# Kernel optimization log

Measured on AMD Instinct MI355X. Metric: run time of the kernel, lower is better.

Reference implementation:

```python
import jax, jax.numpy as jnp
import numpy as np

EPS = 1e-5  # BatchNorm eps

def _bn(x):
    # BatchNorm1d(affine=False) in training mode: per-agent, per-feature batch stats
    m = jnp.mean(x, axis=1, keepdims=True)
    v = jnp.var(x, axis=1, keepdims=True)
    return (x - m) / jnp.sqrt(v + EPS)

def _lrelu(x):
    return jax.nn.leaky_relu(x, 0.01)

def setup_inputs() -> dict:
    key = jax.random.key(0)
    ks = jax.random.split(key, 14)
    A, B, IN, OUT, H, K = 8, 32768, 128, 32, 128, 4
    D = H // K
    s = 0.05
    return {
        "states": jax.random.normal(ks[0], (A, B, IN), jnp.float32),
        "actions": jax.random.normal(ks[1], (A, B, OUT), jnp.float32),
        "enc_w": jax.random.normal(ks[2], (A, IN + OUT, H), jnp.float32) * s,
        "enc_b": jax.random.normal(ks[3], (A, H), jnp.float32) * s,
        "aenc_w": jax.random.normal(ks[4], (A, OUT, H), jnp.float32) * s,
        "aenc_b": jax.random.normal(ks[5], (A, H), jnp.float32) * s,
        "key_w": jax.random.normal(ks[6], (K, H, D), jnp.float32) * s,
        "sel_w": jax.random.normal(ks[7], (K, H, D), jnp.float32) * s,
        "val_w": jax.random.normal(ks[8], (K, H, D), jnp.float32) * s,
        "val_b": jax.random.normal(ks[9], (K, D), jnp.float32) * s,
        "c1_w": jax.random.normal(ks[10], (A, 2 * H, H), jnp.float32) * s,
        "c1_b": jax.random.normal(ks[11], (A, H), jnp.float32) * s,
        "c2_w": jax.random.normal(ks[12], (A, H, 1), jnp.float32) * s,
        "c2_b": jax.random.normal(ks[13], (A, 1), jnp.float32) * s,
    }

def reference(states, actions, enc_w, enc_b, aenc_w, aenc_b,
              key_w, sel_w, val_w, val_b, c1_w, c1_b, c2_w, c2_b):
    A, B, _ = states.shape
    # per-agent state-action encodings: [A,B,H]
    sa = _bn(jnp.concatenate([states, actions], axis=-1))
    sa_enc = _lrelu(jnp.einsum('abi,aih->abh', sa, enc_w) + enc_b[:, None, :])
    # per-agent action encodings: [A,B,H]
    a_in = _bn(actions)
    a_enc = _lrelu(jnp.einsum('abi,aih->abh', a_in, aenc_w) + aenc_b[:, None, :])
    # per-head keys/values/selectors: [K,A,B,D]
    keys = jnp.einsum('abh,khd->kabd', a_enc, key_w)
    vals = _lrelu(jnp.einsum('abh,khd->kabd', a_enc, val_w) + val_b[:, None, None, :])
    sels = jnp.einsum('abh,khd->kabd', sa_enc, sel_w)
    D = keys.shape[-1]
    # attention logits over other agents: [K,B,A_query,A_key], self excluded
    logits = jnp.einsum('kibd,kjbd->kbij', sels, keys) / jnp.sqrt(jnp.float32(D))
    self_mask = jnp.eye(A, dtype=bool)[None, None]
    probs = jax.nn.softmax(jnp.where(self_mask, -jnp.inf, logits), axis=-1)
    # attended values: [K,A,B,D] -> concat heads -> [A,B,K*D]
    other = jnp.einsum('kbij,kjbd->kibd', probs, vals)
    other_cat = jnp.transpose(other, (1, 2, 0, 3)).reshape(A, B, -1)
    # per-agent critics on [sa_enc, attended]: [A,B,1]
    critic_in = jnp.concatenate([sa_enc, other_cat], axis=-1)
    h = _lrelu(jnp.einsum('abi,aih->abh', critic_in, c1_w) + c1_b[:, None, :])
    q = jnp.einsum('abh,aho->abo', h, c2_w) + c2_b[:, None, :]
    return q
```

## Files before the change

kernel.cpp:

```cpp
#include <hip/hip_runtime.h>
#include <hip/hip_bf16.h>
#include <stdint.h>

#define A_N 8
#define B_N 32768
#define IN_N 128
#define OUT_N 32
#define SAF 160
#define H_N 128
#define D_N 32
#define KD_N 128
#define CIN_N 256
#define CHUNKS 128
#define EPSV 1e-5f

typedef unsigned int u32;
typedef unsigned short u16;
typedef __attribute__((ext_vector_type(8))) short short8;
typedef __attribute__((ext_vector_type(4))) float floatx4;

typedef __attribute__((address_space(1))) void gvoid;
typedef __attribute__((address_space(3))) void lvoid;
__device__ __forceinline__ void glds16(const void* g, void* l){
  __builtin_amdgcn_global_load_lds((gvoid*)g, (lvoid*)l, 16, 0, 0);
}

__device__ __forceinline__ int swzu(int u){ return u ^ ((u >> 3) & 3); }
__device__ __forceinline__ int swzi(int rr){
  int u = rr >> 3;
  u ^= (u >> 3) & 3;
  return (u << 3) | (rr & 7);
}

__device__ __forceinline__ float bf_lo(u32 u){ return __uint_as_float(u << 16); }
__device__ __forceinline__ float bf_hi(u32 u){ return __uint_as_float(u & 0xffff0000u); }
__device__ __forceinline__ float bf2f(u16 b){ return __uint_as_float(((u32)b) << 16); }
__device__ __forceinline__ u16 f2bf(float f){
  u32 u = __float_as_uint(f);
  return (u16)((u + 0x7fffu + ((u >> 16) & 1u)) >> 16);
}
__device__ __forceinline__ float lrelu(float x){ return x > 0.f ? x : 0.01f * x; }

__global__ __launch_bounds__(256) void k_stats(
    const float* __restrict__ states, const float* __restrict__ actions,
    float* __restrict__ part)
{
  int a = blockIdx.y;
  int chunk = blockIdx.x;
  int t = threadIdx.x;
  int r0 = chunk * (B_N / CHUNKS);
  __shared__ float red[512];
  {
    int f = t & 127, half = t >> 7;
    const float* p = states + ((size_t)a * B_N + r0 + half) * IN_N + f;
    float s1 = 0.f, s2 = 0.f;
    for (int it = 0; it < 128; ++it){
      float v = p[(size_t)(2 * it) * IN_N];
      s1 += v; s2 += v * v;
    }
    red[t] = s1; red[256 + t] = s2;
    __syncthreads();
    if (t < 128){
      float a1 = red[t] + red[t + 128];
      float a2 = red[256 + t] + red[256 + t + 128];
      size_t o = (((size_t)a * CHUNKS + chunk) * SAF + t) * 2;
      part[o] = a1; part[o + 1] = a2;
    }
    __syncthreads();
  }
  {
    int f = t & 31, g = t >> 5;
    const float* p = actions + ((size_t)a * B_N + r0 + g) * OUT_N + f;
    float s1 = 0.f, s2 = 0.f;
    for (int it = 0; it < 32; ++it){
      float v = p[(size_t)(8 * it) * OUT_N];
      s1 += v; s2 += v * v;
    }
    red[t] = s1; red[256 + t] = s2;
    __syncthreads();
    if (t < 32){
      float a1 = 0.f, a2 = 0.f;
      #pragma unroll
      for (int gg = 0; gg < 8; ++gg){
        a1 += red[t + 32 * gg];
        a2 += red[256 + t + 32 * gg];
      }
      size_t o = (((size_t)a * CHUNKS + chunk) * SAF + 128 + t) * 2;
      part[o] = a1; part[o + 1] = a2;
    }
  }
}

__global__ void k_finalize(const float* __restrict__ part,
                           float* __restrict__ meanArr, float* __restrict__ istdArr)
{
  int idx = blockIdx.x * blockDim.x + threadIdx.x;
  if (idx >= A_N * SAF) return;
  int a = idx / SAF, f = idx % SAF;
  float s1 = 0.f, s2 = 0.f;
  for (int c = 0; c < CHUNKS; ++c){
    size_t o = (((size_t)a * CHUNKS + c) * SAF + f) * 2;
    s1 += part[o]; s2 += part[o + 1];
  }
  float m = s1 * (1.f / B_N);
  float v = s2 * (1.f / B_N) - m * m;
  if (v < 0.f) v = 0.f;
  meanArr[idx] = m;
  istdArr[idx] = rsqrtf(v + EPSV);
}

__device__ __forceinline__ void packpair(float w, u16* __restrict__ dh,
                                         u16* __restrict__ dl, int i){
  u16 h = f2bf(w);
  dh[i] = h;
  dl[i] = f2bf(w - bf2f(h));
}

__global__ __launch_bounds__(256) void k_pack(
    const float* __restrict__ enc_w, const float* __restrict__ aenc_w,
    const float* __restrict__ key_w, const float* __restrict__ sel_w,
    const float* __restrict__ val_w, const float* __restrict__ c1_w,
    u16* __restrict__ encH, u16* __restrict__ encL,
    u16* __restrict__ aencH, u16* __restrict__ aencL,
    u16* __restrict__ keyH, u16* __restrict__ selH, u16* __restrict__ valH,
    u16* __restrict__ c1H, u16* __restrict__ c1L)
{
  int i = blockIdx.x * 256 + threadIdx.x;
  const int S0 = A_N * H_N * SAF;
  const int S1 = A_N * H_N * OUT_N;
  const int S2 = KD_N * H_N;
  const int S5 = A_N * H_N * CIN_N;
  if (i < S0){
    int a = i / (H_N * SAF); int r = i % (H_N * SAF);
    int tile = r >> 12; int rr = r & 4095;
    int n = rr >> 5; int kk = rr & 31;
    int kg = tile * 32 + kk;
    int d = (i & ~4095) | swzi(rr);
    packpair(enc_w[((size_t)a * SAF + kg) * H_N + n], encH, encL, d);
    return;
  }
  i -= S0;
  if (i < S1){
    int a = i >> 12; int rr = i & 4095;
    int n = rr >> 5; int k = rr & 31;
    int d = (i & ~4095) | swzi(rr);
    packpair(aenc_w[((size_t)a * OUT_N + k) * H_N + n], aencH, aencL, d);
    return;
  }
  i -= S1;
  if (i < 3 * S2){
    int which = i / S2; int j = i % S2;
    int tile = j >> 12; int rr = j & 4095;
    int n = rr >> 5; int kk = rr & 31;
    int kg = tile * 32 + kk;
    const float* w = (which == 0) ? key_w : ((which == 1) ? sel_w : val_w);
    u16* dh = (which == 0) ? keyH : ((which == 1) ? selH : valH);
    dh[(j & ~4095) | swzi(rr)] =
        f2bf(w[(((size_t)(n >> 5)) * H_N + kg) * D_N + (n & 31)]);
    return;
  }
  i -= 3 * S2;
  if (i < S5){
    int a = i >> 15; int r = i & 32767;
    int tile = r >> 12; int rr = r & 4095;
    int n = rr >> 5; int kk = rr & 31;
    int kg = tile * 32 + kk;
    int d = (i & ~4095) | swzi(rr);
    packpair(c1_w[((size_t)a * CIN_N + kg) * H_N + n], c1H, c1L, d);
  }
}
#define PACK_TOTAL (A_N*H_N*SAF + A_N*H_N*OUT_N + 3*KD_N*H_N + A_N*H_N*CIN_N)

__global__ __launch_bounds__(256, 3) void k_enc_sel(
    const float* __restrict__ states, const float* __restrict__ actions,
    const float* __restrict__ mean, const float* __restrict__ istd,
    const u16* __restrict__ encH, const u16* __restrict__ encL,
    const float* __restrict__ enc_b,
    const u16* __restrict__ selH,
    u16* __restrict__ sa_enc, u16* __restrict__ sels)
{
  int a = blockIdx.y; int row0 = blockIdx.x * 128; int t = threadIdx.x;
  int lane = t & 63, wave = t >> 6, l16 = lane & 15, quad = lane >> 4;
  __shared__ __align__(16) u16 S[25600];
  __shared__ __align__(16) float sc[160], sh[160];
  u16* Wh = S;
  u16* Wl = S + 4096;
  u16* Xh = S + 8192;
  u16* Xl = S + 13312;
  u16* T  = S;
  u16* Ws = S + 17408;

  if (t < SAF){
    float m = mean[a * SAF + t], s = istd[a * SAF + t];
    sc[t] = s; sh[t] = -m * s;
  }
  floatx4 acc[2][8];
  #pragma unroll
  for (int mt = 0; mt < 2; ++mt)
    #pragma unroll
    for (int nt = 0; nt < 8; ++nt) acc[mt][nt] = (floatx4){0.f,0.f,0.f,0.f};
  const u16* ebh = encH + (size_t)a * (H_N * SAF);
  const u16* ebl = encL + (size_t)a * (H_N * SAF);
  __syncthreads();

  for (int k0 = 0; k0 < SAF; k0 += 32){
    const u16* th = ebh + (k0 >> 5) * 4096;
    const u16* tl = ebl + (k0 >> 5) * 4096;
    #pragma unroll
    for (int c = t; c < 512; c += 256){
      glds16(th + c * 8, Wh + c * 8);
      glds16(tl + c * 8, Wl + c * 8);
    }
    for (int c = t; c < 1024; c += 256){
      int r = c >> 3, kc = (c & 7) * 4, f = k0 + kc;
      size_t row = (size_t)a * B_N + row0 + r;
      float4 v;
      if (f < IN_N) v = *(const float4*)(states + row * IN_N + f);
      else          v = *(const float4*)(actions + row * OUT_N + (f - IN_N));
      float4 scv = *(const float4*)&sc[f];
      float4 shv = *(const float4*)&sh[f];
      float x0 = fmaf(v.x, scv.x, shv.x), x1 = fmaf(v.y, scv.y, shv.y);
      float x2 = fmaf(v.z, scv.z, shv.z), x3 = fmaf(v.w, scv.w, shv.w);
      u16 h0 = f2bf(x0), h1 = f2bf(x1), h2 = f2bf(x2), h3 = f2bf(x3);
      uint2 hv; hv.x = (u32)h0 | ((u32)h1 << 16); hv.y = (u32)h2 | ((u32)h3 << 16);
      *(uint2*)&Xh[r * 40 + kc] = hv;
      u16 l0 = f2bf(x0 - bf2f(h0)), l1 = f2bf(x1 - bf2f(h1));
      u16 l2 = f2bf(x2 - bf2f(h2)), l3 = f2bf(x3 - bf2f(h3));
      uint2 lv; lv.x = (u32)l0 | ((u32)l1 << 16); lv.y = (u32)l2 | ((u32)l3 << 16);
      *(uint2*)&Xl[r * 40 + kc] = lv;
    }
    __syncthreads();
    {
      short8 ah[2], al[2], bh[8], bl[8];
      #pragma unroll
      for (int mt = 0; mt < 2; ++mt){
        int rr = (wave * 32 + mt * 16 + l16) * 40 + quad * 8;
        ah[mt] = *(const short8*)&Xh[rr];
        al[mt] = *(const short8*)&Xl[rr];
      }
      #pragma unroll
      for (int nt = 0; nt < 8; ++nt){
        int v = (nt * 16 + l16) * 4 + quad; v ^= (v >> 3) & 3;
        bh[nt] = *(const short8*)&Wh[v * 8];
        bl[nt] = *(const short8*)&Wl[v * 8];
      }
      #pragma unroll
      for (int mt = 0; mt < 2; ++mt)
        #pragma unroll
        for (int nt = 0; nt < 8; ++nt){
          acc[mt][nt] = __builtin_amdgcn_mfma_f32_16x16x32_bf16(ah[mt], bh[nt], acc[mt][nt], 0,0,0);
          acc[mt][nt] = __builtin_amdgcn_mfma_f32_16x16x32_bf16(ah[mt], bl[nt], acc[mt][nt], 0,0,0);
          acc[mt][nt] = __builtin_amdgcn_mfma_f32_16x16x32_bf16(al[mt], bh[nt], acc[mt][nt], 0,0,0);
        }
    }
    __syncthreads();
  }

  {
    float bv[8];
    #pragma unroll
    for (int nt = 0; nt < 8; ++nt) bv[nt] = enc_b[a * H_N + nt * 16 + l16];
    #pragma unroll
    for (int mt = 0; mt < 2; ++mt)
      #pragma unroll
      for (int nt = 0; nt < 8; ++nt)
        #pragma unroll
        for (int r = 0; r < 4; ++r){
          int rl = wave * 32 + mt * 16 + quad * 4 + r;
          T[rl * 136 + nt * 16 + l16] = f2bf(lrelu(acc[mt][nt][r] + bv[nt]));
        }
  }
  __syncthreads();
  for (int c = t; c < 2048; c += 256){
    int row = c >> 4, col8 = (c & 15) * 8;
    *(uint4*)(sa_enc + ((size_t)a * B_N + row0 + row) * H_N + col8) =
        *(const uint4*)&T[row * 136 + col8];
  }

  #pragma unroll
  for (int mt = 0; mt < 2; ++mt)
    #pragma unroll
    for (int nt = 0; nt < 8; ++nt) acc[mt][nt] = (floatx4){0.f,0.f,0.f,0.f};
  for (int k0 = 0; k0 < H_N; k0 += 64){
    #pragma unroll
    for (int c = t; c < 1024; c += 256)
      glds16(selH + (k0 >> 5) * 4096 + c * 8, Ws + c * 8);
    __syncthreads();
    #pragma unroll
    for (int ks = 0; ks < 64; ks += 32){
      short8 ah[2], bh[8];
      #pragma unroll
      for (int mt = 0; mt < 2; ++mt)
        ah[mt] = *(const short8*)&T[(wave * 32 + mt * 16 + l16) * 136 + k0 + ks + quad * 8];
      #pragma unroll
      for (int nt = 0; nt < 8; ++nt){
        int v = ((ks >> 5) << 9) + (nt * 16 + l16) * 4 + quad; v ^= (v >> 3) & 3;
        bh[nt] = *(const short8*)&Ws[v * 8];
      }
      #pragma unroll
      for (int mt = 0; mt < 2; ++mt)
        #pragma unroll
        for (int nt = 0; nt < 8; ++nt)
          acc[mt][nt] = __builtin_amdgcn_mfma_f32_16x16x32_bf16(ah[mt], bh[nt], acc[mt][nt], 0,0,0);
    }
    __syncthreads();
  }
  #pragma unroll
  for (int mt = 0; mt < 2; ++mt)
    #pragma unroll
    for (int nt = 0; nt < 8; ++nt)
      #pragma unroll
      for (int r = 0; r < 4; ++r){
        int rl = wave * 32 + mt * 16 + quad * 4 + r;
        T[rl * 136 + nt * 16 + l16] = f2bf(acc[mt][nt][r]);
      }
  __syncthreads();
  for (int c = t; c < 2048; c += 256){
    int row = c >> 4, col8 = (c & 15) * 8;
    *(uint4*)(sels + ((size_t)a * B_N + row0 + row) * H_N + col8) =
        *(const uint4*)&T[row * 136 + col8];
  }
}

__global__ __launch_bounds__(256, 2) void k_aenc_kv(
    const float* __restrict__ actions,
    const float* __restrict__ mean, const float* __restrict__ istd,
    const u16* __restrict__ aencH, const u16* __restrict__ aencL,
    const float* __restrict__ aenc_b,
    const u16* __restrict__ keyH, const u16* __restrict__ valH,
    const float* __restrict__ val_b,
    u16* __restrict__ keys, u16* __restrict__ vals)
{
  int a = blockIdx.y; int row0 = blockIdx.x * 128; int t = threadIdx.x;
  int lane = t & 63, wave = t >> 6, l16 = lane & 15, quad = lane >> 4;
  __shared__ __align__(16) u16 S[34816];
  __shared__ __align__(16) float sc[32], sh[32];
  u16* T  = S;
  u16* WK = S + 17408;
  u16* WV = S + 25600;
  u16* T2 = S + 17408;

  if (t < 32){
    float m = mean[a * SAF + 128 + t], s = istd[a * SAF + 128 + t];
    sc[t] = s; sh[t] = -m * s;
  }
  floatx4 accK[2][8], accV[2][8];
  #pragma unroll
  for (int mt = 0; mt < 2; ++mt)
    #pragma unroll
    for (int nt = 0; nt < 8; ++nt){
      accK[mt][nt] = (floatx4){0.f,0.f,0.f,0.f};
      accV[mt][nt] = (floatx4){0.f,0.f,0.f,0.f};
    }
  __syncthreads();

  {
    u16* Wh1 = S;  u16* Wl1 = S + 4096;
    u16* Xh = S + 8192; u16* Xl = S + 13312;
    const u16* abh = aencH + (size_t)a * 4096;
    const u16* abl = aencL + (size_t)a * 4096;
    #pragma unroll
    for (int c = t; c < 512; c += 256){
      glds16(abh + c * 8, Wh1 + c * 8);
      glds16(abl + c * 8, Wl1 + c * 8);
    }
    for (int c = t; c < 1024; c += 256){
      int r = c >> 3, kc = (c & 7) * 4;
      size_t row = (size_t)a * B_N + row0 + r;
      float4 v = *(const float4*)(actions + row * OUT_N + kc);
      float4 scv = *(const float4*)&sc[kc];
      float4 shv = *(const float4*)&sh[kc];
      float x0 = fmaf(v.x, scv.x, shv.x), x1 = fmaf(v.y, scv.y, shv.y);
      float x2 = fmaf(v.z, scv.z, shv.z), x3 = fmaf(v.w, scv.w, shv.w);
      u16 h0 = f2bf(x0), h1 = f2bf(x1), h2 = f2bf(x2), h3 = f2bf(x3);
      uint2 hv; hv.x = (u32)h0 | ((u32)h1 << 16); hv.y = (u32)h2 | ((u32)h3 << 16);
      *(uint2*)&Xh[r * 40 + kc] = hv;
      u16 l0 = f2bf(x0 - bf2f(h0)), l1 = f2bf(x1 - bf2f(h1));
      u16 l2 = f2bf(x2 - bf2f(h2)), l3 = f2bf(x3 - bf2f(h3));
      uint2 lv; lv.x = (u32)l0 | ((u32)l1 << 16); lv.y = (u32)l2 | ((u32)l3 << 16);
      *(uint2*)&Xl[r * 40 + kc] = lv;
    }
    __syncthreads();
    short8 ah[2], al[2], bh[8], bl[8];
    #pragma unroll
    for (int mt = 0; mt < 2; ++mt){
      int rr = (wave * 32 + mt * 16 + l16) * 40 + quad * 8;
      ah[mt] = *(const short8*)&Xh[rr];
      al[mt] = *(const short8*)&Xl[rr];
    }
    #pragma unroll
    for (int nt = 0; nt < 8; ++nt){
      int v = (nt * 16 + l16) * 4 + quad; v ^= (v >> 3) & 3;
      bh[nt] = *(const short8*)&Wh1[v * 8];
      bl[nt] = *(const short8*)&Wl1[v * 8];
    }
    #pragma unroll
    for (int mt = 0; mt < 2; ++mt)
      #pragma unroll
      for (int nt = 0; nt < 8; ++nt){
        accK[mt][nt] = __builtin_amdgcn_mfma_f32_16x16x32_bf16(ah[mt], bh[nt], accK[mt][nt], 0,0,0);
        accK[mt][nt] = __builtin_amdgcn_mfma_f32_16x16x32_bf16(ah[mt], bl[nt], accK[mt][nt], 0,0,0);
        accK[mt][nt] = __builtin_amdgcn_mfma_f32_16x16x32_bf16(al[mt], bh[nt], accK[mt][nt], 0,0,0);
      }
    __syncthreads();
  }
  {
    float bv[8];
    #pragma unroll
    for (int nt = 0; nt < 8; ++nt) bv[nt] = aenc_b[a * H_N + nt * 16 + l16];
    #pragma unroll
    for (int mt = 0; mt < 2; ++mt)
      #pragma unroll
      for (int nt = 0; nt < 8; ++nt){
        #pragma unroll
        for (int r = 0; r < 4; ++r){
          int rl = wave * 32 + mt * 16 + quad * 4 + r;
          T[rl * 136 + nt * 16 + l16] = f2bf(lrelu(accK[mt][nt][r] + bv[nt]));
        }
        accK[mt][nt] = (floatx4){0.f,0.f,0.f,0.f};
      }
  }

  for (int k0 = 0; k0 < H_N; k0 += 64){
    __syncthreads();
    #pragma unroll
    for (int c = t; c < 1024; c += 256){
      glds16(keyH + (k0 >> 5) * 4096 + c * 8, WK + c * 8);
      glds16(valH + (k0 >> 5) * 4096 + c * 8, WV + c * 8);
    }
    __syncthreads();
    #pragma unroll
    for (int ks = 0; ks < 64; ks += 32){
      short8 ah[2], bk[8], bv[8];
      #pragma unroll
      for (int mt = 0; mt < 2; ++mt)
        ah[mt] = *(const short8*)&T[(wave * 32 + mt * 16 + l16) * 136 + k0 + ks + quad * 8];
      #pragma unroll
      for (int nt = 0; nt < 8; ++nt){
        int v = ((ks >> 5) << 9) + (nt * 16 + l16) * 4 + quad; v ^= (v >> 3) & 3;
        bk[nt] = *(const short8*)&WK[v * 8];
        bv[nt] = *(const short8*)&WV[v * 8];
      }
      #pragma unroll
      for (int mt = 0; mt < 2; ++mt)
        #pragma unroll
        for (int nt = 0; nt < 8; ++nt){
          accK[mt][nt] = __builtin_amdgcn_mfma_f32_16x16x32_bf16(ah[mt], bk[nt], accK[mt][nt], 0,0,0);
          accV[mt][nt] = __builtin_amdgcn_mfma_f32_16x16x32_bf16(ah[mt], bv[nt], accV[mt][nt], 0,0,0);
        }
    }
  }
  __syncthreads();
  {
    float bv[8];
    #pragma unroll
    for (int nt = 0; nt < 8; ++nt) bv[nt] = val_b[nt * 16 + l16];
    #pragma unroll
    for (int mt = 0; mt < 2; ++mt)
      #pragma unroll
      for (int nt = 0; nt < 8; ++nt)
        #pragma unroll
        for (int r = 0; r < 4; ++r){
          int rl = wave * 32 + mt * 16 + quad * 4 + r;
          T[rl * 136 + nt * 16 + l16]  = f2bf(lrelu(accV[mt][nt][r] + bv[nt]));
          T2[rl * 136 + nt * 16 + l16] = f2bf(accK[mt][nt][r]);
        }
  }
  __syncthreads();
  for (int c = t; c < 2048; c += 256){
    int row = c >> 4, col8 = (c & 15) * 8;
    *(uint4*)(vals + ((size_t)a * B_N + row0 + row) * H_N + col8) =
        *(const uint4*)&T[row * 136 + col8];
    *(uint4*)(keys + ((size_t)a * B_N + row0 + row) * H_N + col8) =
        *(const uint4*)&T2[row * 136 + col8];
  }
}

__global__ __launch_bounds__(256) void k_attn(
    const u16* __restrict__ sels, const u16* __restrict__ keys,
    const u16* __restrict__ vals, u16* __restrict__ other)
{
  int b0 = blockIdx.x * 8;
  int t = threadIdx.x;
  __shared__ __align__(16) u16 sS[8192], sK[8192], sV[8192];
  #pragma unroll
  for (int c = t; c < 1024; c += 256){
    int pr = c >> 4, uir = c & 15;
    int aa = pr & 7, bl2 = pr >> 3;
    int kk = uir >> 2, dg = uir & 3;
    int U = (bl2 * 4 + dg) * 32 + kk * 8 + (aa ^ (kk << 1) ^ dg);
    size_t go = ((size_t)aa * B_N + b0 + bl2) * KD_N;
    ((uint4*)sS)[U] = *((const uint4*)(sels + go) + uir);
    ((uint4*)sK)[U] = *((const uint4*)(keys + go) + uir);
    ((uint4*)sV)[U] = *((const uint4*)(vals + go) + uir);
  }
  __syncthreads();
  int i = t & 7, k = (t >> 3) & 3, bl = t >> 5;
  float si[32];
  #pragma unroll
  for (int dg = 0; dg < 4; ++dg){
    int U = (bl * 4 + dg) * 32 + k * 8 + (i ^ (k << 1) ^ dg);
    uint4 s4 = ((const uint4*)sS)[U];
    const u32* sp = (const u32*)&s4;
    #pragma unroll
    for (int jj = 0; jj < 4; ++jj){
      int d2 = dg * 4 + jj;
      si[2 * d2] = bf_lo(sp[jj]); si[2 * d2 + 1] = bf_hi(sp[jj]);
    }
  }
  float lg[8];
  #pragma unroll
  for (int j = 0; j < 8; ++j){
    float acc = 0.f;
    #pragma unroll
    for (int dg = 0; dg < 4; ++dg){
      int U = (bl * 4 + dg) * 32 + k * 8 + (j ^ (k << 1) ^ dg);
      uint4 k4 = ((const uint4*)sK)[U];
      const u32* kp = (const u32*)&k4;
      #pragma unroll
      for (int jj = 0; jj < 4; ++jj){
        int d2 = dg * 4 + jj;
        acc = fmaf(si[2 * d2], bf_lo(kp[jj]), acc);
        acc = fmaf(si[2 * d2 + 1], bf_hi(kp[jj]), acc);
      }
    }
    lg[j] = acc * 0.17677669529663689f;
  }
  float mx = -3.0e38f;
  #pragma unroll
  for (int j = 0; j < 8; ++j) if (j != i) mx = fmaxf(mx, lg[j]);
  float pe[8], se = 0.f;
  #pragma unroll
  for (int j = 0; j < 8; ++j){
    pe[j] = (j == i) ? 0.f : __expf(lg[j] - mx);
    se += pe[j];
  }
  float inv = 1.f / se;
  #pragma unroll
  for (int j = 0; j < 8; ++j) pe[j] *= inv;
  float o0[16], o1[16];
  #pragma unroll
  for (int d2 = 0; d2 < 16; ++d2){ o0[d2] = 0.f; o1[d2] = 0.f; }
  #pragma unroll
  for (int j = 0; j < 8; ++j){
    #pragma unroll
    for (int dg = 0; dg < 4; ++dg){
      int U = (bl * 4 + dg) * 32 + k * 8 + (j ^ (k << 1) ^ dg);
      uint4 v4 = ((const uint4*)sV)[U];
      const u32* vp = (const u32*)&v4;
      #pragma unroll
      for (int jj = 0; jj < 4; ++jj){
        int d2 = dg * 4 + jj;
        o0[d2] = fmaf(pe[j], bf_lo(vp[jj]), o0[d2]);
        o1[d2] = fmaf(pe[j], bf_hi(vp[jj]), o1[d2]);
      }
    }
  }
  __align__(16) u16 ob[32];
  #pragma unroll
  for (int d2 = 0; d2 < 16; ++d2){
    ob[2 * d2] = f2bf(o0[d2]); ob[2 * d2 + 1] = f2bf(o1[d2]);
  }
  uint4* dst = (uint4*)(other + ((size_t)i * B_N + (b0 + bl)) * KD_N + k * 32);
  const uint4* s4o = (const uint4*)ob;
  #pragma unroll
  for (int c = 0; c < 4; ++c) dst[c] = s4o[c];
}

__global__ __launch_bounds__(256, 3) void k_critic(
    const u16* __restrict__ sa_enc, const u16* __restrict__ other,
    const u16* __restrict__ c1H, const u16* __restrict__ c1L,
    const float* __restrict__ c1_b,
    const float* __restrict__ c2w, const float* __restrict__ c2b,
    float* __restrict__ qout)
{
  int a = blockIdx.y; int row0 = blockIdx.x * 128; int t = threadIdx.x;
  int lane = t & 63, wave = t >> 6, l16 = lane & 15, quad = lane >> 4;
  __shared__ __align__(16) u16 Xs[4096];
  __shared__ __align__(16) u16 Wh[4096];
  __shared__ __align__(16) u16 Wl[4096];
  floatx4 acc[2][8];
  #pragma unroll
  for (int mt = 0; mt < 2; ++mt)
    #pragma unroll
    for (int nt = 0; nt < 8; ++nt) acc[mt][nt] = (floatx4){0.f,0.f,0.f,0.f};
  const u16* wbh = c1H + (size_t)a * (H_N * CIN_N);
  const u16* wbl = c1L + (size_t)a * (H_N * CIN_N);

  for (int kt = 0; kt < 8; ++kt){
    const u16* th = wbh + kt * 4096;
    const u16* tl = wbl + kt * 4096;
    #pragma unroll
    for (int c = t; c < 512; c += 256){
      glds16(th + c * 8, Wh + c * 8);
      glds16(tl + c * 8, Wl + c * 8);
    }
    {
      const u16* src = (kt < 4) ? sa_enc : other;
      int kb = (kt < 4) ? kt * 32 : kt * 32 - H_N;
      #pragma unroll
      for (int c = t; c < 512; c += 256){
        int r = c >> 2, off = (c & 3) * 8;
        glds16(src + ((size_t)a * B_N + row0 + r) * H_N + kb + off, Xs + c * 8);
      }
    }
    __syncthreads();
    {
      short8 ah[2], bh[8], bl[8];
      #pragma unroll
      for (int mt = 0; mt < 2; ++mt)
        ah[mt] = *(const short8*)&Xs[(wave * 32 + mt * 16 + l16) * 32 + quad * 8];
      #pragma unroll
      for (int nt = 0; nt < 8; ++nt){
        int v = (nt * 16 + l16) * 4 + quad; v ^= (v >> 3) & 3;
        bh[nt] = *(const short8*)&Wh[v * 8];
        bl[nt] = *(const short8*)&Wl[v * 8];
      }
      #pragma unroll
      for (int mt = 0; mt < 2; ++mt)
        #pragma unroll
        for (int nt = 0; nt < 8; ++nt){
          acc[mt][nt] = __builtin_amdgcn_mfma_f32_16x16x32_bf16(ah[mt], bh[nt], acc[mt][nt], 0,0,0);
          acc[mt][nt] = __builtin_amdgcn_mfma_f32_16x16x32_bf16(ah[mt], bl[nt], acc[mt][nt], 0,0,0);
        }
    }
    __syncthreads();
  }

  float c2r[8], bv[8];
  #pragma unroll
  for (int nt = 0; nt < 8; ++nt){
    c2r[nt] = c2w[a * H_N + nt * 16 + l16];
    bv[nt]  = c1_b[a * H_N + nt * 16 + l16];
  }
  #pragma unroll
  for (int mt = 0; mt < 2; ++mt){
    #pragma unroll
    for (int r = 0; r < 4; ++r){
      float s = 0.f;
      #pragma unroll
      for (int nt = 0; nt < 8; ++nt){
        float h = lrelu(acc[mt][nt][r] + bv[nt]);
        s = fmaf(h, c2r[nt], s);
      }
      s += __shfl_xor(s, 1);
      s += __shfl_xor(s, 2);
      s += __shfl_xor(s, 4);
      s += __shfl_xor(s, 8);
      if (l16 == 0){
        int row = row0 + wave * 32 + mt * 16 + quad * 4 + r;
        qout[(size_t)a * B_N + row] = s + c2b[a];
      }
    }
  }
}

extern "C" void kernel_launch(void* const* d_in, const int* in_sizes, int n_in,
                              void* d_out, int out_size, void* d_ws, size_t ws_size,
                              hipStream_t stream)
{
  const float* states  = (const float*)d_in[0];
  const float* actions = (const float*)d_in[1];
  const float* enc_w   = (const float*)d_in[2];
  const float* enc_b   = (const float*)d_in[3];
  const float* aenc_w  = (const float*)d_in[4];
  const float* aenc_b  = (const float*)d_in[5];
  const float* key_w   = (const float*)d_in[6];
  const float* sel_w   = (const float*)d_in[7];
  const float* val_w   = (const float*)d_in[8];
  const float* val_b   = (const float*)d_in[9];
  const float* c1_w    = (const float*)d_in[10];
  const float* c1_b    = (const float*)d_in[11];
  const float* c2_w    = (const float*)d_in[12];
  const float* c2_b    = (const float*)d_in[13];
  float* q = (float*)d_out;

  char* ws = (char*)d_ws;
  u16* encH  = (u16*)(ws + 0);
  u16* encL  = (u16*)(ws + 327680);
  u16* aencH = (u16*)(ws + 655360);
  u16* aencL = (u16*)(ws + 720896);
  u16* keyH  = (u16*)(ws + 786432);
  u16* selH  = (u16*)(ws + 819200);
  u16* valH  = (u16*)(ws + 851968);
  float* part    = (float*)ws;
  float* meanArr = (float*)(ws + 1310720);
  float* istdArr = (float*)(ws + 1315840);
  u16* c1H = (u16*)(ws + 1320960);
  u16* c1L = (u16*)(ws + 1845248);
  const size_t ibase = 4194304;
  const size_t BUF = (size_t)A_N * B_N * 128 * 2;
  u16* sa_enc = (u16*)(ws + ibase);
  u16* sels   = (u16*)(ws + ibase + BUF);
  u16* keys   = (u16*)(ws + ibase + 2 * BUF);
  u16* vals   = (u16*)(ws + ibase + 3 * BUF);

  k_stats<<<dim3(CHUNKS, A_N), 256, 0, stream>>>(states, actions, part);
  k_finalize<<<(A_N * SAF + 255) / 256, 256, 0, stream>>>(part, meanArr, istdArr);
  k_pack<<<(PACK_TOTAL + 255) / 256, 256, 0, stream>>>(
      enc_w, aenc_w, key_w, sel_w, val_w, c1_w,
      encH, encL, aencH, aencL, keyH, selH, valH, c1H, c1L);

  dim3 g(B_N / 128, A_N);
  k_enc_sel<<<g, 256, 0, stream>>>(states, actions, meanArr, istdArr,
                                   encH, encL, enc_b, selH, sa_enc, sels);
  k_aenc_kv<<<g, 256, 0, stream>>>(actions, meanArr, istdArr,
                                   aencH, aencL, aenc_b, keyH, valH, val_b,
                                   keys, vals);
  k_attn<<<B_N / 8, 256, 0, stream>>>(sels, keys, vals, keys);
  k_critic<<<g, 256, 0, stream>>>(sa_enc, keys, c1H, c1L, c1_b, c2_w, c2_b, q);
}
```

Baseline: 509.5 us.

## Drop weight LDS swizzle, shrink aenc_kv LDS, widen critic blocks to 512 threads

```diff
diff --git a/kernel.cpp b/kernel.cpp
--- a/kernel.cpp
+++ b/kernel.cpp
@@ -23,13 +23,6 @@
 typedef __attribute__((address_space(3))) void lvoid;
 __device__ __forceinline__ void glds16(const void* g, void* l){
   __builtin_amdgcn_global_load_lds((gvoid*)g, (lvoid*)l, 16, 0, 0);
-}
-
-__device__ __forceinline__ int swzu(int u){ return u ^ ((u >> 3) & 3); }
-__device__ __forceinline__ int swzi(int rr){
-  int u = rr >> 3;
-  u ^= (u >> 3) & 3;
-  return (u << 3) | (rr & 7);
 }
 
 __device__ __forceinline__ float bf_lo(u32 u){ return __uint_as_float(u << 16); }
@@ -135,16 +128,14 @@
     int tile = r >> 12; int rr = r & 4095;
     int n = rr >> 5; int kk = rr & 31;
     int kg = tile * 32 + kk;
-    int d = (i & ~4095) | swzi(rr);
-    packpair(enc_w[((size_t)a * SAF + kg) * H_N + n], encH, encL, d);
+    packpair(enc_w[((size_t)a * SAF + kg) * H_N + n], encH, encL, i);
     return;
   }
   i -= S0;
   if (i < S1){
     int a = i >> 12; int rr = i & 4095;
     int n = rr >> 5; int k = rr & 31;
-    int d = (i & ~4095) | swzi(rr);
-    packpair(aenc_w[((size_t)a * OUT_N + k) * H_N + n], aencH, aencL, d);
+    packpair(aenc_w[((size_t)a * OUT_N + k) * H_N + n], aencH, aencL, i);
     return;
   }
   i -= S1;
@@ -155,8 +146,7 @@
     int kg = tile * 32 + kk;
     const float* w = (which == 0) ? key_w : ((which == 1) ? sel_w : val_w);
     u16* dh = (which == 0) ? keyH : ((which == 1) ? selH : valH);
-    dh[(j & ~4095) | swzi(rr)] =
-        f2bf(w[(((size_t)(n >> 5)) * H_N + kg) * D_N + (n & 31)]);
+    dh[j] = f2bf(w[(((size_t)(n >> 5)) * H_N + kg) * D_N + (n & 31)]);
     return;
   }
   i -= 3 * S2;
@@ -165,8 +155,7 @@
     int tile = r >> 12; int rr = r & 4095;
     int n = rr >> 5; int kk = rr & 31;
     int kg = tile * 32 + kk;
-    int d = (i & ~4095) | swzi(rr);
-    packpair(c1_w[((size_t)a * CIN_N + kg) * H_N + n], c1H, c1L, d);
+    packpair(c1_w[((size_t)a * CIN_N + kg) * H_N + n], c1H, c1L, i);
   }
 }
 #define PACK_TOTAL (A_N*H_N*SAF + A_N*H_N*OUT_N + 3*KD_N*H_N + A_N*H_N*CIN_N)
@@ -240,9 +229,9 @@
       }
       #pragma unroll
       for (int nt = 0; nt < 8; ++nt){
-        int v = (nt * 16 + l16) * 4 + quad; v ^= (v >> 3) & 3;
-        bh[nt] = *(const short8*)&Wh[v * 8];
-        bl[nt] = *(const short8*)&Wl[v * 8];
+        int rr = (nt * 16 + l16) * 32 + quad * 8;
+        bh[nt] = *(const short8*)&Wh[rr];
+        bl[nt] = *(const short8*)&Wl[rr];
       }
       #pragma unroll
       for (int mt = 0; mt < 2; ++mt)
@@ -293,10 +282,8 @@
       for (int mt = 0; mt < 2; ++mt)
         ah[mt] = *(const short8*)&T[(wave * 32 + mt * 16 + l16) * 136 + k0 + ks + quad * 8];
       #pragma unroll
-      for (int nt = 0; nt < 8; ++nt){
-        int v = ((ks >> 5) << 9) + (nt * 16 + l16) * 4 + quad; v ^= (v >> 3) & 3;
-        bh[nt] = *(const short8*)&Ws[v * 8];
-      }
+      for (int nt = 0; nt < 8; ++nt)
+        bh[nt] = *(const short8*)&Ws[((ks >> 5) << 12) + (nt * 16 + l16) * 32 + quad * 8];
       #pragma unroll
       for (int mt = 0; mt < 2; ++mt)
         #pragma unroll
@@ -322,7 +309,7 @@
   }
 }
 
-__global__ __launch_bounds__(256, 2) void k_aenc_kv(
+__global__ __launch_bounds__(256, 3) void k_aenc_kv(
     const float* __restrict__ actions,
     const float* __restrict__ mean, const float* __restrict__ istd,
     const u16* __restrict__ aencH, const u16* __restrict__ aencL,
@@ -333,12 +320,11 @@
 {
   int a = blockIdx.y; int row0 = blockIdx.x * 128; int t = threadIdx.x;
   int lane = t & 63, wave = t >> 6, l16 = lane & 15, quad = lane >> 4;
-  __shared__ __align__(16) u16 S[34816];
+  __shared__ __align__(16) u16 S[25600];
   __shared__ __align__(16) float sc[32], sh[32];
   u16* T  = S;
   u16* WK = S + 17408;
-  u16* WV = S + 25600;
-  u16* T2 = S + 17408;
+  u16* WV = S + 21504;
 
   if (t < 32){
     float m = mean[a * SAF + 128 + t], s = istd[a * SAF + 128 + t];
@@ -390,9 +376,9 @@
     }
     #pragma unroll
     for (int nt = 0; nt < 8; ++nt){
-      int v = (nt * 16 + l16) * 4 + quad; v ^= (v >> 3) & 3;
-      bh[nt] = *(const short8*)&Wh1[v * 8];
-      bl[nt] = *(const short8*)&Wl1[v * 8];
+      int rr = (nt * 16 + l16) * 32 + quad * 8;
+      bh[nt] = *(const short8*)&Wh1[rr];
+      bl[nt] = *(const short8*)&Wl1[rr];
     }
     #pragma unroll
     for (int mt = 0; mt < 2; ++mt)
@@ -421,25 +407,24 @@
       }
   }
 
-  for (int k0 = 0; k0 < H_N; k0 += 64){
-    __syncthreads();
-    #pragma unroll
-    for (int c = t; c < 1024; c += 256){
+  for (int k0 = 0; k0 < H_N; k0 += 32){
+    __syncthreads();
+    #pragma unroll
+    for (int c = t; c < 512; c += 256){
       glds16(keyH + (k0 >> 5) * 4096 + c * 8, WK + c * 8);
       glds16(valH + (k0 >> 5) * 4096 + c * 8, WV + c * 8);
     }
     __syncthreads();
-    #pragma unroll
-    for (int ks = 0; ks < 64; ks += 32){
+    {
       short8 ah[2], bk[8], bv[8];
       #pragma unroll
       for (int mt = 0; mt < 2; ++mt)
-        ah[mt] = *(const short8*)&T[(wave * 32 + mt * 16 + l16) * 136 + k0 + ks + quad * 8];
+        ah[mt] = *(const short8*)&T[(wave * 32 + mt * 16 + l16) * 136 + k0 + quad * 8];
       #pragma unroll
       for (int nt = 0; nt < 8; ++nt){
-        int v = ((ks >> 5) << 9) + (nt * 16 + l16) * 4 + quad; v ^= (v >> 3) & 3;
-        bk[nt] = *(const short8*)&WK[v * 8];
-        bv[nt] = *(const short8*)&WV[v * 8];
+        int rr = (nt * 16 + l16) * 32 + quad * 8;
+        bk[nt] = *(const short8*)&WK[rr];
+        bv[nt] = *(const short8*)&WV[rr];
       }
       #pragma unroll
       for (int mt = 0; mt < 2; ++mt)
@@ -462,8 +447,7 @@
         #pragma unroll
         for (int r = 0; r < 4; ++r){
           int rl = wave * 32 + mt * 16 + quad * 4 + r;
-          T[rl * 136 + nt * 16 + l16]  = f2bf(lrelu(accV[mt][nt][r] + bv[nt]));
-          T2[rl * 136 + nt * 16 + l16] = f2bf(accK[mt][nt][r]);
+          T[rl * 136 + nt * 16 + l16] = f2bf(lrelu(accV[mt][nt][r] + bv[nt]));
         }
   }
   __syncthreads();
@@ -471,8 +455,22 @@
     int row = c >> 4, col8 = (c & 15) * 8;
     *(uint4*)(vals + ((size_t)a * B_N + row0 + row) * H_N + col8) =
         *(const uint4*)&T[row * 136 + col8];
+  }
+  __syncthreads();
+  #pragma unroll
+  for (int mt = 0; mt < 2; ++mt)
+    #pragma unroll
+    for (int nt = 0; nt < 8; ++nt)
+      #pragma unroll
+      for (int r = 0; r < 4; ++r){
+        int rl = wave * 32 + mt * 16 + quad * 4 + r;
+        T[rl * 136 + nt * 16 + l16] = f2bf(accK[mt][nt][r]);
+      }
+  __syncthreads();
+  for (int c = t; c < 2048; c += 256){
+    int row = c >> 4, col8 = (c & 15) * 8;
     *(uint4*)(keys + ((size_t)a * B_N + row0 + row) * H_N + col8) =
-        *(const uint4*)&T2[row * 136 + col8];
+        *(const uint4*)&T[row * 136 + col8];
   }
 }
 
@@ -567,16 +565,16 @@
   for (int c = 0; c < 4; ++c) dst[c] = s4o[c];
 }
 
-__global__ __launch_bounds__(256, 3) void k_critic(
+__global__ __launch_bounds__(512, 4) void k_critic(
     const u16* __restrict__ sa_enc, const u16* __restrict__ other,
     const u16* __restrict__ c1H, const u16* __restrict__ c1L,
     const float* __restrict__ c1_b,
     const float* __restrict__ c2w, const float* __restrict__ c2b,
     float* __restrict__ qout)
 {
-  int a = blockIdx.y; int row0 = blockIdx.x * 128; int t = threadIdx.x;
+  int a = blockIdx.y; int row0 = blockIdx.x * 256; int t = threadIdx.x;
   int lane = t & 63, wave = t >> 6, l16 = lane & 15, quad = lane >> 4;
-  __shared__ __align__(16) u16 Xs[4096];
+  __shared__ __align__(16) u16 Xs[8192];
   __shared__ __align__(16) u16 Wh[4096];
   __shared__ __align__(16) u16 Wl[4096];
   floatx4 acc[2][8];
@@ -590,16 +588,18 @@
   for (int kt = 0; kt < 8; ++kt){
     const u16* th = wbh + kt * 4096;
     const u16* tl = wbl + kt * 4096;
-    #pragma unroll
-    for (int c = t; c < 512; c += 256){
-      glds16(th + c * 8, Wh + c * 8);
-      glds16(tl + c * 8, Wl + c * 8);
+    {
+      int c = t;
+      if (c < 512){
+        glds16(th + c * 8, Wh + c * 8);
+        glds16(tl + c * 8, Wl + c * 8);
+      }
     }
     {
       const u16* src = (kt < 4) ? sa_enc : other;
       int kb = (kt < 4) ? kt * 32 : kt * 32 - H_N;
       #pragma unroll
-      for (int c = t; c < 512; c += 256){
+      for (int c = t; c < 1024; c += 512){
         int r = c >> 2, off = (c & 3) * 8;
         glds16(src + ((size_t)a * B_N + row0 + r) * H_N + kb + off, Xs + c * 8);
       }
@@ -612,9 +612,9 @@
         ah[mt] = *(const short8*)&Xs[(wave * 32 + mt * 16 + l16) * 32 + quad * 8];
       #pragma unroll
       for (int nt = 0; nt < 8; ++nt){
-        int v = (nt * 16 + l16) * 4 + quad; v ^= (v >> 3) & 3;
-        bh[nt] = *(const short8*)&Wh[v * 8];
-        bl[nt] = *(const short8*)&Wl[v * 8];
+        int rr = (nt * 16 + l16) * 32 + quad * 8;
+        bh[nt] = *(const short8*)&Wh[rr];
+        bl[nt] = *(const short8*)&Wl[rr];
       }
       #pragma unroll
       for (int mt = 0; mt < 2; ++mt)
@@ -708,5 +708,6 @@
                                    aencH, aencL, aenc_b, keyH, valH, val_b,
                                    keys, vals);
   k_attn<<<B_N / 8, 256, 0, stream>>>(sels, keys, vals, keys);
-  k_critic<<<g, 256, 0, stream>>>(sa_enc, keys, c1H, c1L, c1_b, c2_w, c2_b, q);
-}
+  dim3 gc(B_N / 256, A_N);
+  k_critic<<<gc, 512, 0, stream>>>(sa_enc, keys, c1H, c1L, c1_b, c2_w, c2_b, q);
+}
```

Result: slower. 666.7 us (+30.8%).
